# Optimization experiments

Measured on AMD Instinct MI355X. Metric: run time of the kernel, lower is better.

Reference implementation:

```python
import jax, jax.numpy as jnp
import numpy as np

TAU = 0.7
# Dellar moment flip under x<->y swap: (rho, jy, jx, Pyy, Pxy, Pxx, N, Jy, Jx)
FLIP = np.array([0, 2, 1, 5, 4, 3, 6, 8, 7])


def _dellar_matrices():
    # D2Q9 velocities in lettuce stencil order
    e = np.array([[0, 0], [1, 0], [0, 1], [-1, 0], [0, -1],
                  [1, 1], [-1, 1], [-1, -1], [1, -1]], dtype=np.float64)
    ex, ey = e[:, 0], e[:, 1]
    g = np.array([1, -2, -2, -2, -2, 4, 4, 4, 4], dtype=np.float64)  # Dellar ghost mode
    third = 1.0 / 3.0
    M = np.stack([
        np.ones(9),            # rho
        ex,                    # jx
        ey,                    # jy
        ex * ex - third,       # Pxx - cs^2 rho
        ex * ey,               # Pxy
        ey * ey - third,       # Pyy - cs^2 rho
        g,                     # N (ghost)
        g * ex,                # Jx (ghost)
        g * ey,                # Jy (ghost)
    ])
    return M, np.linalg.inv(M)


def _mlp(x, w1, b1, w2, b2):
    # x: (nx, ny, 9) -> (nx, ny, 1); Linear(9,24) + ReLU + Linear(24,1)
    h = jax.nn.relu(jnp.einsum('xyi,oi->xyo', x, w1) + b1)
    return jnp.einsum('xyo,po->xyp', h, w2) + b2


def setup_inputs() -> dict:
    key = jax.random.key(0)
    ks = jax.random.split(key, 9)
    nx = ny = 2048
    f = jax.random.uniform(ks[0], (9, nx, ny), dtype=jnp.float32)

    def lin_w(k, o, i):
        return jax.random.uniform(k, (o, i), dtype=jnp.float32,
                                  minval=-1.0, maxval=1.0) / np.sqrt(i)

    def lin_b(k, o, i):
        return jax.random.uniform(k, (o,), dtype=jnp.float32,
                                  minval=-1.0, maxval=1.0) / np.sqrt(i)

    M, Minv = _dellar_matrices()
    return {
        'f': f,
        'j_w1': lin_w(ks[1], 24, 9), 'j_b1': lin_b(ks[2], 24, 9),
        'j_w2': lin_w(ks[3], 1, 24), 'j_b2': lin_b(ks[4], 1, 24),
        'n_w1': lin_w(ks[5], 24, 9), 'n_b1': lin_b(ks[6], 24, 9),
        'n_w2': lin_w(ks[7], 1, 24), 'n_b2': lin_b(ks[8], 1, 24),
        'M': jnp.asarray(M, jnp.float32),
        'Minv': jnp.asarray(Minv, jnp.float32),
    }


def reference(f, j_w1, j_b1, j_w2, j_b2, n_w1, n_b1, n_w2, n_b2, M, Minv):
    # moment transform: m_i = M_ij f_j, shape (9, nx, ny)
    m = jnp.einsum('ij,jxy->ixy', M, f)
    mt = jnp.transpose(m, (1, 2, 0))        # (nx, ny, 9)
    mtf = mt[..., FLIP]                     # x<->y flipped moments

    gt_half = lambda a: 0.5 + jnp.exp(a)
    tau_jx = gt_half(_mlp(mt, j_w1, j_b1, j_w2, j_b2))[..., 0]
    tau_jy = gt_half(_mlp(mtf, j_w1, j_b1, j_w2, j_b2))[..., 0]
    tau_n = gt_half(_mlp(mt, n_w1, n_b1, n_w2, n_b2)
                    + _mlp(mtf, n_w1, n_b1, n_w2, n_b2))[..., 0]

    taus = jnp.full_like(m, TAU)
    taus = taus.at[6].set(tau_n).at[7].set(tau_jx).at[8].set(tau_jy)

    rho, jx, jy = m[0], m[1], m[2]
    zero = jnp.zeros_like(rho)
    meq = jnp.stack([rho, jx, jy,
                     jx * jx / rho, jx * jy / rho, jy * jy / rho,
                     zero, zero, zero])

    m_post = m - (m - meq) / taus
    return jnp.einsum('ij,jxy->ixy', Minv, m_post)
```

## Files before the change

### kernel.cpp

```cpp
#include <hip/hip_runtime.h>

#define TILE 4

__global__ __launch_bounds__(256) void mrt_kernel(
    const float* __restrict__ f,
    const float* __restrict__ j_w1, const float* __restrict__ j_b1,
    const float* __restrict__ j_w2, const float* __restrict__ j_b2,
    const float* __restrict__ n_w1, const float* __restrict__ n_b1,
    const float* __restrict__ n_w2, const float* __restrict__ n_b2,
    const float* __restrict__ Mg, const float* __restrict__ Minvg,
    float* __restrict__ out, int n2)
{
    __shared__ float sW1[24][9][4];
    __shared__ float sMt[9][9];
    __shared__ float sMinv[9][9];
    __shared__ float sB[24][4];
    __shared__ float sb2[2];

    const int tid = threadIdx.x;
    const int FLIPc[9] = {0, 2, 1, 5, 4, 3, 6, 8, 7};

    for (int t = tid; t < 216; t += 256) {
        int o = t / 9, i = t % 9;
        float wj = j_w1[t], wn = n_w1[t];
        sW1[o][i][0] = wj;
        sW1[o][i][2] = wn;
        sW1[o][FLIPc[i]][1] = wj;
        sW1[o][FLIPc[i]][3] = wn;
    }
    for (int t = tid; t < 81; t += 256) {
        int r = t / 9, c = t % 9;
        sMt[c][r]   = Mg[t];
        sMinv[r][c] = Minvg[t];
    }
    if (tid < 24) {
        sB[tid][0] = j_b1[tid];
        sB[tid][1] = n_b1[tid];
        sB[tid][2] = j_w2[tid];
        sB[tid][3] = n_w2[tid];
    }
    if (tid == 0) { sb2[0] = j_b2[0]; sb2[1] = n_b2[0]; }
    __syncthreads();

    const long base = ((long)blockIdx.x * blockDim.x + tid) * TILE;
    if (base >= n2) return;

    float m[9][TILE];
    #pragma unroll
    for (int r = 0; r < 9; ++r)
        #pragma unroll
        for (int k = 0; k < TILE; ++k) m[r][k] = 0.0f;

    #pragma unroll
    for (int i = 0; i < 9; ++i) {
        float4 v = *reinterpret_cast<const float4*>(f + (size_t)i * n2 + base);
        float vv[TILE] = {v.x, v.y, v.z, v.w};
        #pragma unroll
        for (int r = 0; r < 9; ++r) {
            float w = sMt[i][r];
            #pragma unroll
            for (int k = 0; k < TILE; ++k)
                m[r][k] = fmaf(w, vv[k], m[r][k]);
        }
    }

    float aj[TILE], ajf[TILE], an1[TILE], an2[TILE];
    #pragma unroll
    for (int k = 0; k < TILE; ++k) { aj[k] = 0.f; ajf[k] = 0.f; an1[k] = 0.f; an2[k] = 0.f; }

    #pragma unroll 3
    for (int o = 0; o < 24; ++o) {
        float b1j_ = sB[o][0], b1n_ = sB[o][1];
        float hj[TILE], hjf[TILE], hn[TILE], hnf[TILE];
        #pragma unroll
        for (int k = 0; k < TILE; ++k) { hj[k] = b1j_; hjf[k] = b1j_; hn[k] = b1n_; hnf[k] = b1n_; }
        #pragma unroll
        for (int i = 0; i < 9; ++i) {
            float wj  = sW1[o][i][0];
            float wjf = sW1[o][i][1];
            float wn  = sW1[o][i][2];
            float wnf = sW1[o][i][3];
            #pragma unroll
            for (int k = 0; k < TILE; ++k) {
                float x = m[i][k];
                hj[k]  = fmaf(wj,  x, hj[k]);
                hjf[k] = fmaf(wjf, x, hjf[k]);
                hn[k]  = fmaf(wn,  x, hn[k]);
                hnf[k] = fmaf(wnf, x, hnf[k]);
            }
        }
        float w2j_ = sB[o][2], w2n_ = sB[o][3];
        #pragma unroll
        for (int k = 0; k < TILE; ++k) {
            aj[k]  = fmaf(fmaxf(hj[k],  0.f), w2j_, aj[k]);
            ajf[k] = fmaf(fmaxf(hjf[k], 0.f), w2j_, ajf[k]);
            an1[k] = fmaf(fmaxf(hn[k],  0.f), w2n_, an1[k]);
            an2[k] = fmaf(fmaxf(hnf[k], 0.f), w2n_, an2[k]);
        }
    }

    const float b2j_ = sb2[0], b2n_ = sb2[1];

    #pragma unroll
    for (int k = 0; k < TILE; ++k) {
        float tjx = 0.5f + expf(aj[k]  + b2j_);
        float tjy = 0.5f + expf(ajf[k] + b2j_);
        float tn  = 0.5f + expf((an1[k] + b2n_) + (an2[k] + b2n_));

        float rho = m[0][k], jx = m[1][k], jy = m[2][k];
        m[3][k] = m[3][k] - (m[3][k] - jx * jx / rho) / 0.7f;
        m[4][k] = m[4][k] - (m[4][k] - jx * jy / rho) / 0.7f;
        m[5][k] = m[5][k] - (m[5][k] - jy * jy / rho) / 0.7f;
        m[6][k] = m[6][k] - m[6][k] / tn;
        m[7][k] = m[7][k] - m[7][k] / tjx;
        m[8][k] = m[8][k] - m[8][k] / tjy;
    }

    #pragma unroll
    for (int r = 0; r < 9; ++r) {
        float o0[TILE];
        #pragma unroll
        for (int k = 0; k < TILE; ++k) o0[k] = 0.0f;
        #pragma unroll
        for (int j = 0; j < 9; ++j) {
            float w = sMinv[r][j];
            #pragma unroll
            for (int k = 0; k < TILE; ++k)
                o0[k] = fmaf(w, m[j][k], o0[k]);
        }
        float4 vv = make_float4(o0[0], o0[1], o0[2], o0[3]);
        *reinterpret_cast<float4*>(out + (size_t)r * n2 + base) = vv;
    }
}

extern "C" void kernel_launch(void* const* d_in, const int* in_sizes, int n_in,
                              void* d_out, int out_size, void* d_ws, size_t ws_size,
                              hipStream_t stream) {
    const float* f    = (const float*)d_in[0];
    const float* j_w1 = (const float*)d_in[1];
    const float* j_b1 = (const float*)d_in[2];
    const float* j_w2 = (const float*)d_in[3];
    const float* j_b2 = (const float*)d_in[4];
    const float* n_w1 = (const float*)d_in[5];
    const float* n_b1 = (const float*)d_in[6];
    const float* n_w2 = (const float*)d_in[7];
    const float* n_b2 = (const float*)d_in[8];
    const float* Mg   = (const float*)d_in[9];
    const float* Minv = (const float*)d_in[10];
    float* out = (float*)d_out;

    const int n2 = in_sizes[0] / 9;
    const int pts_per_block = 256 * TILE;
    const int grid = (n2 + pts_per_block - 1) / pts_per_block;

    mrt_kernel<<<grid, 256, 0, stream>>>(f, j_w1, j_b1, j_w2, j_b2,
                                         n_w1, n_b1, n_w2, n_b2,
                                         Mg, Minv, out, n2);
}
```

Before: 329.4 us.

## Exploit flip symmetry in MLP and use packed FP32 math

```diff
diff --git a/kernel.cpp b/kernel.cpp
--- a/kernel.cpp
+++ b/kernel.cpp
@@ -1,6 +1,13 @@
 #include <hip/hip_runtime.h>
 
-#define TILE 4
+typedef float f32x2 __attribute__((ext_vector_type(2)));
+
+__device__ __forceinline__ f32x2 splat2(float s) { f32x2 v; v.x = s; v.y = s; return v; }
+__device__ __forceinline__ f32x2 pfma(f32x2 a, f32x2 b, f32x2 c) { return __builtin_elementwise_fma(a, b, c); }
+__device__ __forceinline__ f32x2 pfmas(float a, f32x2 b, f32x2 c) { return __builtin_elementwise_fma(splat2(a), b, c); }
+__device__ __forceinline__ f32x2 prelu(f32x2 a) { return __builtin_elementwise_max(a, splat2(0.0f)); }
+
+#define NP 2
 
 __global__ __launch_bounds__(256) void mrt_kernel(
     const float* __restrict__ f,
@@ -11,124 +18,144 @@
     const float* __restrict__ Mg, const float* __restrict__ Minvg,
     float* __restrict__ out, int n2)
 {
-    __shared__ float sW1[24][9][4];
+    __shared__ __align__(16) float sW[24][20];
+    __shared__ float sW2[24][2];
     __shared__ float sMt[9][9];
-    __shared__ float sMinv[9][9];
-    __shared__ float sB[24][4];
+    __shared__ float sMv[9][9];
     __shared__ float sb2[2];
 
     const int tid = threadIdx.x;
-    const int FLIPc[9] = {0, 2, 1, 5, 4, 3, 6, 8, 7};
 
-    for (int t = tid; t < 216; t += 256) {
-        int o = t / 9, i = t % 9;
-        float wj = j_w1[t], wn = n_w1[t];
-        sW1[o][i][0] = wj;
-        sW1[o][i][2] = wn;
-        sW1[o][FLIPc[i]][1] = wj;
-        sW1[o][FLIPc[i]][3] = wn;
+    if (tid < 48) {
+        const int o = tid >> 1;
+        const int which = tid & 1;
+        const float* w1 = which ? n_w1 : j_w1;
+        const float* b1 = which ? n_b1 : j_b1;
+        float w[9];
+        #pragma unroll
+        for (int i = 0; i < 9; ++i) w[i] = w1[o * 9 + i];
+        float* dst = &sW[o][which * 10];
+        dst[0] = w[0]; dst[1] = w[4]; dst[2] = w[6];
+        dst[3] = 0.5f * (w[1] + w[2]); dst[4] = 0.5f * (w[3] + w[5]); dst[5] = 0.5f * (w[7] + w[8]);
+        dst[6] = 0.5f * (w[1] - w[2]); dst[7] = 0.5f * (w[3] - w[5]); dst[8] = 0.5f * (w[7] - w[8]);
+        dst[9] = b1[o];
+        if (which == 0) { sW2[o][0] = j_w2[o]; sW2[o][1] = n_w2[o]; }
     }
     for (int t = tid; t < 81; t += 256) {
-        int r = t / 9, c = t % 9;
-        sMt[c][r]   = Mg[t];
-        sMinv[r][c] = Minvg[t];
-    }
-    if (tid < 24) {
-        sB[tid][0] = j_b1[tid];
-        sB[tid][1] = n_b1[tid];
-        sB[tid][2] = j_w2[tid];
-        sB[tid][3] = n_w2[tid];
+        sMt[t % 9][t / 9] = Mg[t];
+        sMv[t / 9][t % 9] = Minvg[t];
     }
     if (tid == 0) { sb2[0] = j_b2[0]; sb2[1] = n_b2[0]; }
     __syncthreads();
 
-    const long base = ((long)blockIdx.x * blockDim.x + tid) * TILE;
+    const long base = ((long)blockIdx.x * blockDim.x + tid) * (2 * NP);
     if (base >= n2) return;
 
-    float m[9][TILE];
+    f32x2 m[NP][9];
     #pragma unroll
-    for (int r = 0; r < 9; ++r)
+    for (int p = 0; p < NP; ++p)
         #pragma unroll
-        for (int k = 0; k < TILE; ++k) m[r][k] = 0.0f;
+        for (int r = 0; r < 9; ++r) m[p][r] = splat2(0.0f);
 
     #pragma unroll
     for (int i = 0; i < 9; ++i) {
-        float4 v = *reinterpret_cast<const float4*>(f + (size_t)i * n2 + base);
-        float vv[TILE] = {v.x, v.y, v.z, v.w};
+        const float4 v = *reinterpret_cast<const float4*>(f + (size_t)i * n2 + base);
+        f32x2 v0; v0.x = v.x; v0.y = v.y;
+        f32x2 v1; v1.x = v.z; v1.y = v.w;
         #pragma unroll
         for (int r = 0; r < 9; ++r) {
-            float w = sMt[i][r];
-            #pragma unroll
-            for (int k = 0; k < TILE; ++k)
-                m[r][k] = fmaf(w, vv[k], m[r][k]);
+            const float w = sMt[i][r];
+            m[0][r] = pfmas(w, v0, m[0][r]);
+            m[1][r] = pfmas(w, v1, m[1][r]);
         }
     }
 
-    float aj[TILE], ajf[TILE], an1[TILE], an2[TILE];
+    f32x2 tv[NP][9];
     #pragma unroll
-    for (int k = 0; k < TILE; ++k) { aj[k] = 0.f; ajf[k] = 0.f; an1[k] = 0.f; an2[k] = 0.f; }
+    for (int p = 0; p < NP; ++p) {
+        tv[p][0] = m[p][0]; tv[p][1] = m[p][4]; tv[p][2] = m[p][6];
+        tv[p][3] = m[p][1] + m[p][2]; tv[p][4] = m[p][3] + m[p][5]; tv[p][5] = m[p][7] + m[p][8];
+        tv[p][6] = m[p][1] - m[p][2]; tv[p][7] = m[p][3] - m[p][5]; tv[p][8] = m[p][7] - m[p][8];
+    }
 
-    #pragma unroll 3
+    f32x2 accj[NP], accjf[NP], accn[NP];
+    #pragma unroll
+    for (int p = 0; p < NP; ++p) { accj[p] = splat2(0.f); accjf[p] = splat2(0.f); accn[p] = splat2(0.f); }
+
+    #pragma unroll 4
     for (int o = 0; o < 24; ++o) {
-        float b1j_ = sB[o][0], b1n_ = sB[o][1];
-        float hj[TILE], hjf[TILE], hn[TILE], hnf[TILE];
+        const float4* pw = reinterpret_cast<const float4*>(sW[o]);
+        const float4 c0 = pw[0], c1 = pw[1], c2 = pw[2], c3 = pw[3], c4 = pw[4];
+        const float w2j = sW2[o][0], w2n = sW2[o][1];
         #pragma unroll
-        for (int k = 0; k < TILE; ++k) { hj[k] = b1j_; hjf[k] = b1j_; hn[k] = b1n_; hnf[k] = b1n_; }
-        #pragma unroll
-        for (int i = 0; i < 9; ++i) {
-            float wj  = sW1[o][i][0];
-            float wjf = sW1[o][i][1];
-            float wn  = sW1[o][i][2];
-            float wnf = sW1[o][i][3];
-            #pragma unroll
-            for (int k = 0; k < TILE; ++k) {
-                float x = m[i][k];
-                hj[k]  = fmaf(wj,  x, hj[k]);
-                hjf[k] = fmaf(wjf, x, hjf[k]);
-                hn[k]  = fmaf(wn,  x, hn[k]);
-                hnf[k] = fmaf(wnf, x, hnf[k]);
-            }
-        }
-        float w2j_ = sB[o][2], w2n_ = sB[o][3];
-        #pragma unroll
-        for (int k = 0; k < TILE; ++k) {
-            aj[k]  = fmaf(fmaxf(hj[k],  0.f), w2j_, aj[k]);
-            ajf[k] = fmaf(fmaxf(hjf[k], 0.f), w2j_, ajf[k]);
-            an1[k] = fmaf(fmaxf(hn[k],  0.f), w2n_, an1[k]);
-            an2[k] = fmaf(fmaxf(hnf[k], 0.f), w2n_, an2[k]);
+        for (int p = 0; p < NP; ++p) {
+            f32x2 s = splat2(c2.y);
+            s = pfmas(c0.x, tv[p][0], s);
+            s = pfmas(c0.y, tv[p][1], s);
+            s = pfmas(c0.z, tv[p][2], s);
+            s = pfmas(c0.w, tv[p][3], s);
+            s = pfmas(c1.x, tv[p][4], s);
+            s = pfmas(c1.y, tv[p][5], s);
+            f32x2 a = splat2(c1.z) * tv[p][6];
+            a = pfmas(c1.w, tv[p][7], a);
+            a = pfmas(c2.x, tv[p][8], a);
+            const f32x2 hj  = prelu(s + a);
+            const f32x2 hjf = prelu(s - a);
+
+            f32x2 sn = splat2(c4.w);
+            sn = pfmas(c2.z, tv[p][0], sn);
+            sn = pfmas(c2.w, tv[p][1], sn);
+            sn = pfmas(c3.x, tv[p][2], sn);
+            sn = pfmas(c3.y, tv[p][3], sn);
+            sn = pfmas(c3.z, tv[p][4], sn);
+            sn = pfmas(c3.w, tv[p][5], sn);
+            f32x2 an_ = splat2(c4.x) * tv[p][6];
+            an_ = pfmas(c4.y, tv[p][7], an_);
+            an_ = pfmas(c4.z, tv[p][8], an_);
+            const f32x2 hn  = prelu(sn + an_);
+            const f32x2 hnf = prelu(sn - an_);
+
+            accj[p]  = pfmas(w2j, hj,  accj[p]);
+            accjf[p] = pfmas(w2j, hjf, accjf[p]);
+            accn[p]  = pfmas(w2n, hn + hnf, accn[p]);
         }
     }
 
-    const float b2j_ = sb2[0], b2n_ = sb2[1];
-
+    const float b2j = sb2[0], b2n = sb2[1];
+    const f32x2 Cs = splat2(1.0f / 0.7f);
     #pragma unroll
-    for (int k = 0; k < TILE; ++k) {
-        float tjx = 0.5f + expf(aj[k]  + b2j_);
-        float tjy = 0.5f + expf(ajf[k] + b2j_);
-        float tn  = 0.5f + expf((an1[k] + b2n_) + (an2[k] + b2n_));
-
-        float rho = m[0][k], jx = m[1][k], jy = m[2][k];
-        m[3][k] = m[3][k] - (m[3][k] - jx * jx / rho) / 0.7f;
-        m[4][k] = m[4][k] - (m[4][k] - jx * jy / rho) / 0.7f;
-        m[5][k] = m[5][k] - (m[5][k] - jy * jy / rho) / 0.7f;
-        m[6][k] = m[6][k] - m[6][k] / tn;
-        m[7][k] = m[7][k] - m[7][k] / tjx;
-        m[8][k] = m[8][k] - m[8][k] / tjy;
+    for (int p = 0; p < NP; ++p) {
+        const f32x2 aj  = accj[p]  + splat2(b2j);
+        const f32x2 ajf = accjf[p] + splat2(b2j);
+        const f32x2 an  = accn[p]  + splat2(2.0f * b2n);
+        f32x2 rt7, rt8, rt6, rrho;
+        rt7.x = __builtin_amdgcn_rcpf(0.5f + __expf(aj.x));
+        rt7.y = __builtin_amdgcn_rcpf(0.5f + __expf(aj.y));
+        rt8.x = __builtin_amdgcn_rcpf(0.5f + __expf(ajf.x));
+        rt8.y = __builtin_amdgcn_rcpf(0.5f + __expf(ajf.y));
+        rt6.x = __builtin_amdgcn_rcpf(0.5f + __expf(an.x));
+        rt6.y = __builtin_amdgcn_rcpf(0.5f + __expf(an.y));
+        rrho.x = __builtin_amdgcn_rcpf(m[p][0].x);
+        rrho.y = __builtin_amdgcn_rcpf(m[p][0].y);
+        const f32x2 jx = m[p][1], jy = m[p][2];
+        m[p][3] = m[p][3] - (m[p][3] - jx * jx * rrho) * Cs;
+        m[p][4] = m[p][4] - (m[p][4] - jx * jy * rrho) * Cs;
+        m[p][5] = m[p][5] - (m[p][5] - jy * jy * rrho) * Cs;
+        m[p][6] = m[p][6] - m[p][6] * rt6;
+        m[p][7] = m[p][7] - m[p][7] * rt7;
+        m[p][8] = m[p][8] - m[p][8] * rt8;
     }
 
     #pragma unroll
     for (int r = 0; r < 9; ++r) {
-        float o0[TILE];
-        #pragma unroll
-        for (int k = 0; k < TILE; ++k) o0[k] = 0.0f;
+        f32x2 o0 = splat2(0.f), o1 = splat2(0.f);
         #pragma unroll
         for (int j = 0; j < 9; ++j) {
-            float w = sMinv[r][j];
-            #pragma unroll
-            for (int k = 0; k < TILE; ++k)
-                o0[k] = fmaf(w, m[j][k], o0[k]);
+            const float w = sMv[r][j];
+            o0 = pfmas(w, m[0][j], o0);
+            o1 = pfmas(w, m[1][j], o1);
         }
-        float4 vv = make_float4(o0[0], o0[1], o0[2], o0[3]);
+        const float4 vv = make_float4(o0.x, o0.y, o1.x, o1.y);
         *reinterpret_cast<float4*>(out + (size_t)r * n2 + base) = vv;
     }
 }
@@ -150,7 +177,7 @@
     float* out = (float*)d_out;
 
     const int n2 = in_sizes[0] / 9;
-    const int pts_per_block = 256 * TILE;
+    const int pts_per_block = 256 * 2 * NP;
     const int grid = (n2 + pts_per_block - 1) / pts_per_block;
 
     mrt_kernel<<<grid, 256, 0, stream>>>(f, j_w1, j_b1, j_w2, j_b2,
```

After: 300.2 us. -8.9%, faster.
